# Performance work log

Hardware: AMD Instinct MI355X
Metric: run time of the kernel (lower is better)

Reference implementation:

```python
import jax, jax.numpy as jnp
import numpy as np
from jax.scipy.special import gammaln

BIG_NEG = -1e9
MAX_K = 20  # args.sm_max_span_length


def setup_inputs() -> dict:
    key = jax.random.key(0)
    ks = jax.random.split(key, 7)
    B, N, d, C = 16, 2048, 256, 128
    features = jax.random.normal(ks[0], (B, N, d), dtype=jnp.float32)
    lengths = jax.random.randint(ks[1], (B,), N // 2, N + 1)
    gaussian_means = jax.random.normal(ks[2], (C, d), dtype=jnp.float32)
    cov_diag = jax.random.uniform(ks[3], (d,), minval=0.5, maxval=1.5, dtype=jnp.float32)
    transition_logits = jax.random.normal(ks[4], (C, C), dtype=jnp.float32)
    init_logits = jax.random.uniform(ks[5], (C,), dtype=jnp.float32)
    poisson_log_rates = jax.random.normal(ks[6], (C,), dtype=jnp.float32) * 0.5 + 1.5
    return {"features": features, "lengths": lengths, "gaussian_means": gaussian_means,
            "cov_diag": cov_diag, "transition_logits": transition_logits,
            "init_logits": init_logits, "poisson_log_rates": poisson_log_rates}


def _emission_log_probs(features, means, cov_diag):
    # Diagonal-covariance MultivariateNormal log-prob, one class per column.
    # Quadratic form expanded to avoid materializing [B,N,C,d].
    inv_var = 1.0 / cov_diag
    d = features.shape[-1]
    const = -0.5 * (d * jnp.log(2.0 * jnp.pi) + jnp.sum(jnp.log(cov_diag)))
    xq = jnp.einsum('bnd,d->bn', features * features, inv_var)          # [B,N]
    mq = jnp.einsum('cd,d->c', means * means, inv_var)                  # [C]
    xm = jnp.einsum('bnd,cd->bnc', features, means * inv_var)           # [B,N,C]
    return const - 0.5 * (xq[..., None] + mq[None, None, :] - 2.0 * xm)  # [B,N,C]


def _length_log_probs(log_rates, K):
    # Poisson log-prob for span lengths k = 1..K.
    ks = jnp.arange(1, K + 1, dtype=jnp.float32)[:, None]               # [K,1]
    return ks * log_rates[None, :] - jnp.exp(log_rates)[None, :] - gammaln(ks + 1.0)  # [K,C]


def _transition_log_probs(transition_logits):
    C = transition_logits.shape[0]
    masked = jnp.where(jnp.eye(C, dtype=bool), BIG_NEG, transition_logits)  # no self-transitions
    return jax.nn.log_softmax(masked, axis=0)  # normalized over destination class (dim 0)


def _semimarkov_logZ(emis_lp, lengths, init_lp, trans_lp, len_lp, K):
    # Segmental (semi-Markov) CRF forward algorithm with sliding-window span sums.
    B, N, C = emis_lp.shape
    cum = jnp.concatenate([jnp.zeros((B, 1, C), emis_lp.dtype), jnp.cumsum(emis_lp, axis=1)], axis=1)
    cum_pad = jnp.concatenate([jnp.zeros((B, K, C), emis_lp.dtype), cum], axis=1)  # idx t+K <-> position t
    beta0 = jnp.full((B, N + 1 + K, C), BIG_NEG, emis_lp.dtype)
    beta0 = beta0.at[:, K, :].set(init_lp[None, :])  # position 0: initial distribution
    len_rev = len_lp[::-1]  # len_rev[j] == length log-prob of span length K-j

    def step(beta, t):
        w = jax.lax.dynamic_slice(beta, (0, t, 0), (B, K, C))        # beta at positions t-K..t-1
        cw = jax.lax.dynamic_slice(cum_pad, (0, t, 0), (B, K, C))
        ct = jax.lax.dynamic_slice(cum_pad, (0, t + K, 0), (B, 1, C))
        span = w + len_rev[None, :, :] + (ct - cw)                    # [B,K,C] span scores ending at t
        alpha_t = jax.nn.logsumexp(span, axis=1)                      # [B,C]
        beta_t = jax.nn.logsumexp(alpha_t[:, None, :] + trans_lp[None, :, :], axis=2)  # to-class
        beta = jax.lax.dynamic_update_slice(beta, beta_t[:, None, :], (0, t + K, 0))
        return beta, alpha_t

    _, alphas = jax.lax.scan(step, beta0, jnp.arange(1, N + 1))       # alphas: [N,B,C]
    final = alphas[lengths - 1, jnp.arange(B)]                        # [B,C] at each sequence end
    return jax.nn.logsumexp(final, axis=1)                            # [B] log partition


def reference(features, lengths, gaussian_means, cov_diag, transition_logits, init_logits, poisson_log_rates):
    emis_lp = _emission_log_probs(features, gaussian_means, cov_diag)
    init_lp = jax.nn.log_softmax(init_logits, axis=0)
    trans_lp = _transition_log_probs(transition_logits)
    len_lp = _length_log_probs(poisson_log_rates, MAX_K)
    return _semimarkov_logZ(emis_lp, lengths, init_lp, trans_lp, len_lp, MAX_K)
```

## Files before the change

### kernel.cpp

```cpp
#include <hip/hip_runtime.h>
#include <math.h>

#define Bb 16
#define Nn 2048
#define Dd 256
#define Cc 128
#define Kk 20
#define BIG_NEG -1.0e9f

#define WS_EMIS   0
#define WS_MSC    (WS_EMIS + Bb*Nn*Cc)
#define WS_XQ     (WS_MSC + Cc*Dd)
#define WS_ECHAN  (WS_XQ + Bb*Nn)
#define WS_T      (WS_ECHAN + Cc)
#define WS_LEN    (WS_T + Cc*Cc)
#define WS_INIT   (WS_LEN + Kk*Cc)
#define WS_IVAR   (WS_INIT + Cc)

typedef __attribute__((ext_vector_type(8))) short short8;
typedef __attribute__((ext_vector_type(4))) float float4v;

__device__ __forceinline__ unsigned short f32_to_bf16(float x) {
  unsigned int u = __builtin_bit_cast(unsigned int, x);
  u = (u + 0x7FFFu + ((u >> 16) & 1u)) >> 16;
  return (unsigned short)u;
}

#define DPP_STEP(x, op, ctrl, rmask)                                          \
  do {                                                                        \
    int _yi = __builtin_amdgcn_update_dpp(                                    \
        __builtin_bit_cast(int, x), __builtin_bit_cast(int, x), ctrl, rmask,  \
        0xF, true);                                                           \
    x = op(x, __builtin_bit_cast(float, _yi));                                \
  } while (0)

__device__ __forceinline__ float dpp_add(float a, float b) { return a + b; }

__device__ __forceinline__ float wave_max64(float x) {
  DPP_STEP(x, fmaxf, 0xB1, 0xF);
  DPP_STEP(x, fmaxf, 0x4E, 0xF);
  DPP_STEP(x, fmaxf, 0x141, 0xF);
  DPP_STEP(x, fmaxf, 0x140, 0xF);
  DPP_STEP(x, fmaxf, 0x142, 0xA);
  DPP_STEP(x, fmaxf, 0x143, 0xC);
  return __builtin_bit_cast(float,
      __builtin_amdgcn_readlane(__builtin_bit_cast(int, x), 63));
}

__device__ __forceinline__ float wave_sum64(float x) {
  DPP_STEP(x, dpp_add, 0xB1, 0xF);
  DPP_STEP(x, dpp_add, 0x4E, 0xF);
  DPP_STEP(x, dpp_add, 0x141, 0xF);
  DPP_STEP(x, dpp_add, 0x140, 0xF);
  DPP_STEP(x, dpp_add, 0x142, 0xA);
  DPP_STEP(x, dpp_add, 0x143, 0xC);
  return __builtin_bit_cast(float,
      __builtin_amdgcn_readlane(__builtin_bit_cast(int, x), 63));
}

__global__ void prep_kernel(const float* __restrict__ means,
                            const float* __restrict__ cov,
                            const float* __restrict__ tl,
                            const float* __restrict__ il,
                            const float* __restrict__ plr,
                            float* __restrict__ ws) {
  __shared__ float s_iv[Dd];
  __shared__ float s_red[4];
  __shared__ float s_tlse[Cc];
  int tid = threadIdx.x;

  float cv = cov[tid];
  float iv = 1.0f / cv;
  s_iv[tid] = iv;
  ws[WS_IVAR + tid] = iv;
  float lg = __logf(cv);
  #pragma unroll
  for (int off = 1; off < 64; off <<= 1) lg += __shfl_xor(lg, off, 64);
  if ((tid & 63) == 0) s_red[tid >> 6] = lg;
  __syncthreads();
  float logdet = s_red[0] + s_red[1] + s_red[2] + s_red[3];
  float cconst = -0.5f * ((float)Dd * 1.8378770664093453f + logdet);

  unsigned short* mscb = (unsigned short*)(ws + WS_MSC);
  for (int idx = tid; idx < Cc * Dd; idx += 256) {
    int d = idx & (Dd - 1);
    mscb[idx] = f32_to_bf16(means[idx] * s_iv[d]);
  }
  if (tid < Cc) {
    float acc = 0.0f;
    for (int d = 0; d < Dd; d++) {
      float m = means[tid * Dd + d];
      acc = fmaf(m * m, s_iv[d], acc);
    }
    ws[WS_ECHAN + tid] = cconst - 0.5f * acc;
  }
  for (int idx = tid; idx < Kk * Cc; idx += 256) {
    int L = idx / Cc + 1;
    int c = idx & (Cc - 1);
    float r = plr[c];
    ws[WS_LEN + idx] = (float)L * r - __expf(r) - lgammaf((float)(L + 1));
  }

  __syncthreads();
  float x = (tid < Cc) ? il[tid] : -INFINITY;
  float mx = x;
  #pragma unroll
  for (int off = 1; off < 64; off <<= 1) mx = fmaxf(mx, __shfl_xor(mx, off, 64));
  if ((tid & 63) == 0) s_red[tid >> 6] = mx;
  __syncthreads();
  float M = fmaxf(s_red[0], s_red[1]);
  float se = (tid < Cc) ? __expf(x - M) : 0.0f;
  #pragma unroll
  for (int off = 1; off < 64; off <<= 1) se += __shfl_xor(se, off, 64);
  __syncthreads();
  if ((tid & 63) == 0) s_red[tid >> 6] = se;
  __syncthreads();
  float lse = M + __logf(s_red[0] + s_red[1]);
  if (tid < Cc) ws[WS_INIT + tid] = x - lse;

  if (tid < Cc) {
    int j = tid;
    float m2 = -INFINITY;
    for (int i = 0; i < Cc; i++) if (i != j) m2 = fmaxf(m2, tl[i * Cc + j]);
    float s2 = 0.0f;
    for (int i = 0; i < Cc; i++) if (i != j) s2 += __expf(tl[i * Cc + j] - m2);
    s_tlse[j] = m2 + __logf(s2);
  }
  __syncthreads();
  for (int idx = tid; idx < Cc * Cc; idx += 256) {
    int i = idx / Cc;
    int j = idx & (Cc - 1);
    ws[WS_T + idx] = (i == j) ? 0.0f : __expf(tl[idx] - s_tlse[j]);
  }
}

__global__ void xq_kernel(const float* __restrict__ f, float* __restrict__ ws) {
  int pos = blockIdx.x * 4 + (threadIdx.x >> 6);
  int lane = threadIdx.x & 63;
  const float4 fv = *(const float4*)&f[(size_t)pos * Dd + lane * 4];
  const float4 vv = *(const float4*)&ws[WS_IVAR + lane * 4];
  float a = fv.x * fv.x * vv.x + fv.y * fv.y * vv.y +
            fv.z * fv.z * vv.z + fv.w * fv.w * vv.w;
  #pragma unroll
  for (int off = 1; off < 64; off <<= 1) a += __shfl_xor(a, off, 64);
  if (lane == 0) ws[WS_XQ + pos] = a;
}

__launch_bounds__(256)
__global__ void emis_mfma_kernel(const float* __restrict__ f, float* __restrict__ ws) {
  const unsigned short* msc = (const unsigned short*)(ws + WS_MSC);
  float* emis = ws + WS_EMIS;
  int tid = threadIdx.x;
  int w = tid >> 6, lane = tid & 63, g = lane >> 4, l16 = lane & 15;
  int b = blockIdx.x >> 6;
  int n0 = (blockIdx.x & 63) << 5;
  int c0 = w << 5;

  const float* fbase = f + (size_t)(b * Nn + n0) * Dd;
  float4v acc[2][2];
  #pragma unroll
  for (int rt = 0; rt < 2; rt++)
    #pragma unroll
    for (int ct = 0; ct < 2; ct++) acc[rt][ct] = (float4v){0.f, 0.f, 0.f, 0.f};

  #pragma unroll
  for (int k0 = 0; k0 < Dd; k0 += 32) {
    int kk = k0 + g * 8;
    short8 afr[2], bfr[2];
    #pragma unroll
    for (int rt = 0; rt < 2; rt++) {
      const float* src = fbase + (size_t)(rt * 16 + l16) * Dd + kk;
      float4 v0 = *(const float4*)src;
      float4 v1 = *(const float4*)(src + 4);
      short8 fr;
      fr[0] = (short)f32_to_bf16(v0.x); fr[1] = (short)f32_to_bf16(v0.y);
      fr[2] = (short)f32_to_bf16(v0.z); fr[3] = (short)f32_to_bf16(v0.w);
      fr[4] = (short)f32_to_bf16(v1.x); fr[5] = (short)f32_to_bf16(v1.y);
      fr[6] = (short)f32_to_bf16(v1.z); fr[7] = (short)f32_to_bf16(v1.w);
      afr[rt] = fr;
    }
    #pragma unroll
    for (int ct = 0; ct < 2; ct++)
      bfr[ct] = *(const short8*)&msc[(size_t)(c0 + ct * 16 + l16) * Dd + kk];
    #pragma unroll
    for (int rt = 0; rt < 2; rt++)
      #pragma unroll
      for (int ct = 0; ct < 2; ct++)
        acc[rt][ct] = __builtin_amdgcn_mfma_f32_16x16x32_bf16(afr[rt], bfr[ct], acc[rt][ct], 0, 0, 0);
  }

  #pragma unroll
  for (int rt = 0; rt < 2; rt++) {
    #pragma unroll
    for (int ct = 0; ct < 2; ct++) {
      int cc = c0 + ct * 16 + l16;
      float ec = ws[WS_ECHAN + cc];
      #pragma unroll
      for (int r = 0; r < 4; r++) {
        int row = rt * 16 + g * 4 + r;
        int nn = n0 + row;
        emis[(size_t)(b * Nn + nn) * Cc + cc] =
            ec - 0.5f * ws[WS_XQ + b * Nn + nn] + acc[rt][ct][r];
      }
    }
  }
}

__launch_bounds__(128, 1)
__global__ void scan_kernel(const int* __restrict__ lengths,
                            const float* __restrict__ ws,
                            float* __restrict__ out) {
  __shared__ __align__(16) unsigned short p_lds[2][Cc];
  __shared__ float lds_wv[2][2];
  __shared__ float lds_men[2][2][8];
  __shared__ float lds_out[2][2];

  int tid = threadIdx.x;
  int w = tid >> 6;
  int lane = tid & 63;
  int g = lane >> 4;
  int l15 = lane & 15;
  int c = w * 64 + lane;
  int b = blockIdx.x;
  int len_b = lengths[b];
  const float* emis = ws + WS_EMIS + (size_t)b * Nn * Cc;

  short8 Tf[4][4];
  {
    const float* T = ws + WS_T;
    #pragma unroll
    for (int nt = 0; nt < 4; nt++)
      #pragma unroll
      for (int kc = 0; kc < 4; kc++) {
        const float* src = &T[(size_t)((w * 4 + nt) * 16 + l15) * Cc + kc * 32 + g * 8];
        short8 fr;
        #pragma unroll
        for (int j = 0; j < 8; j++) fr[j] = (short)f32_to_bf16(src[j]);
        Tf[nt][kc] = fr;
      }
  }

  float elen[Kk];
  #pragma unroll
  for (int k = 0; k < Kk; k++) elen[k] = __expf(ws[WS_LEN + k * Cc + c]);
  float elen0 = elen[0];

  float E[Kk - 1];
  #pragma unroll
  for (int s = 0; s < Kk - 1; s++) E[s] = 0.0f;

  float q = __expf(ws[WS_INIT + c]);
  float Stail = 0.0f;
  float cum = 0.0f;
  float Dlt = 0.0f, dcomp = 0.0f;

  float e[8], en[8];
  #pragma unroll
  for (int j = 0; j < 8; j++) e[j] = emis[(size_t)j * Cc + c];
  #pragma unroll
  for (int j = 0; j < 8; j++) {
    float m = wave_max64(e[j]);
    if (lane == 0) lds_men[0][w][j] = m;
  }
  __syncthreads();
  float ee = __expf(e[0] - fmaxf(lds_men[0][0][0], lds_men[0][1][0]));

  bool done = false;
  for (int tg = 1; tg <= Nn && !done; tg += 8) {
    int gp = ((tg - 1) >> 3) & 1;
    #pragma unroll
    for (int i = 0; i < 8; i++) {
      int t = tg + i;
      int buf = t & 1;
      bool fin = (t == len_b);
      float ecur = e[i];
      float S = fmaf(q, elen0, Stail);
      float a = 0.0f;

      if (fin) {
        a = (cum + ecur) + Dlt + __logf(fmaxf(S, 1e-37f));
        float Mw = wave_max64(a);
        if (lane == 0) lds_out[0][w] = Mw;
      } else {
        float v = S * ee;
        p_lds[buf][c] = f32_to_bf16(v);
        float wvp = wave_max64(v);
        if (lane == 0) lds_wv[buf][w] = wvp;
      }
      __syncthreads();

      if (fin) {
        float Mb = fmaxf(lds_out[0][0], lds_out[0][1]);
        float ps = wave_sum64(__expf(a - Mb));
        if (lane == 0) lds_out[1][w] = ps;
        __syncthreads();
        if (tid == 0) out[b] = Mb + __logf(lds_out[1][0] + lds_out[1][1]);
        done = true;
        break;
      }

      short8 pa0 = *(const short8*)&p_lds[buf][g * 8];
      short8 pa1 = *(const short8*)&p_lds[buf][32 + g * 8];
      short8 pa2 = *(const short8*)&p_lds[buf][64 + g * 8];
      short8 pa3 = *(const short8*)&p_lds[buf][96 + g * 8];
      float wv = fmaxf(fmaxf(lds_wv[buf][0], lds_wv[buf][1]), 1.0e-30f);
      float r = __builtin_amdgcn_rcpf(wv);

      if (i == 0) {
        #pragma unroll
        for (int j = 0; j < 8; j++) {
          int rr = tg + 7 + j;
          if (rr > Nn - 1) rr = Nn - 1;
          en[j] = emis[(size_t)rr * Cc + c];
        }
      }

      float4v z = {0.0f, 0.0f, 0.0f, 0.0f};
      float qv[4];
      #pragma unroll
      for (int nt = 0; nt < 4; nt++) {
        float4v x = __builtin_amdgcn_mfma_f32_16x16x32_bf16(pa1, Tf[nt][1],
                      __builtin_amdgcn_mfma_f32_16x16x32_bf16(pa0, Tf[nt][0], z, 0, 0, 0),
                      0, 0, 0);
        float4v y = __builtin_amdgcn_mfma_f32_16x16x32_bf16(pa3, Tf[nt][3],
                      __builtin_amdgcn_mfma_f32_16x16x32_bf16(pa2, Tf[nt][2], z, 0, 0, 0),
                      0, 0, 0);
        qv[nt] = x[0] + y[0];
      }

      float sch = ee * r;
      #pragma unroll
      for (int s = Kk - 2; s >= 1; s--) E[s] = E[s - 1] * sch;
      E[0] = q * sch;

      float s0 = E[0] * elen[1];
      float s1 = E[1] * elen[2];
      float s2 = E[2] * elen[3];
      float s3 = E[3] * elen[4];
      s0 = fmaf(E[4], elen[5], s0);   s1 = fmaf(E[5], elen[6], s1);
      s2 = fmaf(E[6], elen[7], s2);   s3 = fmaf(E[7], elen[8], s3);
      s0 = fmaf(E[8], elen[9], s0);   s1 = fmaf(E[9], elen[10], s1);
      s2 = fmaf(E[10], elen[11], s2); s3 = fmaf(E[11], elen[12], s3);
      s0 = fmaf(E[12], elen[13], s0); s1 = fmaf(E[13], elen[14], s1);
      s2 = fmaf(E[14], elen[15], s2); s3 = fmaf(E[15], elen[16], s3);
      s0 = fmaf(E[16], elen[17], s0); s1 = fmaf(E[17], elen[18], s1);
      s2 = fmaf(E[18], elen[19], s2);
      Stail = (s0 + s1) + (s2 + s3);

      float meC = fmaxf(lds_men[gp][0][i], lds_men[gp][1][i]);
      float dla = meC + __logf(wv);
      {
        float dd = dla - ecur;
        float yk = dd - dcomp;
        float t2 = Dlt + yk;
        dcomp = (t2 - Dlt) - yk;
        Dlt = t2;
      }
      cum += ecur;

      if (i >= 2) {
        float m = wave_max64(en[i - 2]);
        if (lane == 0) lds_men[gp ^ 1][w][i - 2] = m;
      }
      if (i == 6) {
        float m = wave_max64(en[6]);
        if (lane == 0) lds_men[gp ^ 1][w][6] = m;
      }
      if (i == 7) {
        float m = wave_max64(en[7]);
        if (lane == 0) lds_men[gp ^ 1][w][7] = m;
      }

      if (i < 7) {
        float meN = fmaxf(lds_men[gp][0][i + 1], lds_men[gp][1][i + 1]);
        ee = __expf(e[i + 1] - meN);
      }

      float qs01 = (g & 1) ? qv[1] : qv[0];
      float qs23 = (g & 1) ? qv[3] : qv[2];
      float qs = (g & 2) ? qs23 : qs01;
      q = qs * r;
    }
    if (!done) {
      #pragma unroll
      for (int j = 0; j < 8; j++) e[j] = en[j];
      int gp = ((tg - 1) >> 3) & 1;
      float me0 = fmaxf(lds_men[gp ^ 1][0][0], lds_men[gp ^ 1][1][0]);
      ee = __expf(e[0] - me0);
    }
  }
}

extern "C" void kernel_launch(void* const* d_in, const int* in_sizes, int n_in,
                              void* d_out, int out_size, void* d_ws, size_t ws_size,
                              hipStream_t stream) {
  const float* features = (const float*)d_in[0];
  const int* lengths = (const int*)d_in[1];
  const float* means = (const float*)d_in[2];
  const float* cov = (const float*)d_in[3];
  const float* tl = (const float*)d_in[4];
  const float* il = (const float*)d_in[5];
  const float* plr = (const float*)d_in[6];
  float* out = (float*)d_out;
  float* ws = (float*)d_ws;

  prep_kernel<<<1, 256, 0, stream>>>(means, cov, tl, il, plr, ws);
  xq_kernel<<<(Bb * Nn) / 4, 256, 0, stream>>>(features, ws);
  emis_mfma_kernel<<<Bb * (Nn / 32), 256, 0, stream>>>(features, ws);
  scan_kernel<<<Bb, 128, 0, stream>>>(lengths, ws, out);
}
```

Measured before the change: 1.559 ms.

## Derive per-step normalizer from bf16 LDS fragments and defer rescale to next step

The scan no longer does a wave max reduction plus an LDS exchange for the normalizer each step. Each wave recomputes the max from the bf16 probability fragments it already reads for the MFMA, via packed u16 max and a short DPP tail. The reciprocal and log of that normalizer are folded into the next step's emission scale, which takes them off the critical path. __syncthreads is replaced by a raw s_waitcnt+s_barrier, bf16 conversion becomes plain truncation, and emission prefetch loads are spread across the 8 substeps. The risks are extra bf16 truncation error and rescaling that is delayed by one step.

```diff
diff --git a/kernel.cpp b/kernel.cpp
--- a/kernel.cpp
+++ b/kernel.cpp
@@ -19,6 +19,9 @@
 
 typedef __attribute__((ext_vector_type(8))) short short8;
 typedef __attribute__((ext_vector_type(4))) float float4v;
+typedef __attribute__((ext_vector_type(8))) unsigned short u16x8;
+typedef __attribute__((ext_vector_type(4))) unsigned short u16x4;
+typedef __attribute__((ext_vector_type(2))) unsigned short u16x2;
 
 __device__ __forceinline__ unsigned short f32_to_bf16(float x) {
   unsigned int u = __builtin_bit_cast(unsigned int, x);
@@ -56,6 +59,32 @@
   DPP_STEP(x, dpp_add, 0x143, 0xC);
   return __builtin_bit_cast(float,
       __builtin_amdgcn_readlane(__builtin_bit_cast(int, x), 63));
+}
+
+#define WAVE_BARRIER() asm volatile("s_waitcnt lgkmcnt(0)\n\ts_barrier" ::: "memory")
+
+__device__ __forceinline__ float frag_max_to_f32(short8 a, short8 b, short8 c, short8 d) {
+  u16x8 ua = __builtin_bit_cast(u16x8, a), ub = __builtin_bit_cast(u16x8, b);
+  u16x8 uc = __builtin_bit_cast(u16x8, c), ud = __builtin_bit_cast(u16x8, d);
+  u16x8 m8 = __builtin_elementwise_max(__builtin_elementwise_max(ua, ub),
+                                       __builtin_elementwise_max(uc, ud));
+  u16x4 lo4 = __builtin_shufflevector(m8, m8, 0, 1, 2, 3);
+  u16x4 hi4 = __builtin_shufflevector(m8, m8, 4, 5, 6, 7);
+  u16x4 m4 = __builtin_elementwise_max(lo4, hi4);
+  u16x2 lo2 = __builtin_shufflevector(m4, m4, 0, 1);
+  u16x2 hi2 = __builtin_shufflevector(m4, m4, 2, 3);
+  u16x2 m2 = __builtin_elementwise_max(lo2, hi2);
+  unsigned mm = (unsigned)m2[0];
+  unsigned m1 = (unsigned)m2[1];
+  mm = mm > m1 ? mm : m1;
+  {
+    int y = __builtin_amdgcn_update_dpp((int)mm, (int)mm, 0x142, 0xA, 0xF, true);
+    unsigned uy = (unsigned)y; mm = mm > uy ? mm : uy;
+    y = __builtin_amdgcn_update_dpp((int)mm, (int)mm, 0x143, 0xC, 0xF, true);
+    uy = (unsigned)y; mm = mm > uy ? mm : uy;
+  }
+  unsigned full = (unsigned)__builtin_amdgcn_readlane((int)mm, 63);
+  return __builtin_bit_cast(float, full << 16);
 }
 
 __global__ void prep_kernel(const float* __restrict__ means,
@@ -211,7 +240,6 @@
                             const float* __restrict__ ws,
                             float* __restrict__ out) {
   __shared__ __align__(16) unsigned short p_lds[2][Cc];
-  __shared__ float lds_wv[2][2];
   __shared__ float lds_men[2][2][8];
   __shared__ float lds_out[2][2];
 
@@ -253,6 +281,8 @@
   float Stail = 0.0f;
   float cum = 0.0f;
   float Dlt = 0.0f, dcomp = 0.0f;
+  float r = 1.0f;
+  float lwv = 0.0f;
 
   float e[8], en[8];
   #pragma unroll
@@ -262,8 +292,8 @@
     float m = wave_max64(e[j]);
     if (lane == 0) lds_men[0][w][j] = m;
   }
-  __syncthreads();
-  float ee = __expf(e[0] - fmaxf(lds_men[0][0][0], lds_men[0][1][0]));
+  WAVE_BARRIER();
+  float eesc = __expf(e[0] - fmaxf(lds_men[0][0][0], lds_men[0][1][0]));
 
   bool done = false;
   for (int tg = 1; tg <= Nn && !done; tg += 8) {
@@ -282,18 +312,17 @@
         float Mw = wave_max64(a);
         if (lane == 0) lds_out[0][w] = Mw;
       } else {
-        float v = S * ee;
-        p_lds[buf][c] = f32_to_bf16(v);
-        float wvp = wave_max64(v);
-        if (lane == 0) lds_wv[buf][w] = wvp;
-      }
-      __syncthreads();
+        float v = S * eesc;
+        p_lds[buf][c] =
+            (unsigned short)(__builtin_bit_cast(unsigned int, v) >> 16);
+      }
+      WAVE_BARRIER();
 
       if (fin) {
         float Mb = fmaxf(lds_out[0][0], lds_out[0][1]);
         float ps = wave_sum64(__expf(a - Mb));
         if (lane == 0) lds_out[1][w] = ps;
-        __syncthreads();
+        WAVE_BARRIER();
         if (tid == 0) out[b] = Mb + __logf(lds_out[1][0] + lds_out[1][1]);
         done = true;
         break;
@@ -303,17 +332,20 @@
       short8 pa1 = *(const short8*)&p_lds[buf][32 + g * 8];
       short8 pa2 = *(const short8*)&p_lds[buf][64 + g * 8];
       short8 pa3 = *(const short8*)&p_lds[buf][96 + g * 8];
-      float wv = fmaxf(fmaxf(lds_wv[buf][0], lds_wv[buf][1]), 1.0e-30f);
-      float r = __builtin_amdgcn_rcpf(wv);
 
       if (i == 0) {
-        #pragma unroll
-        for (int j = 0; j < 8; j++) {
-          int rr = tg + 7 + j;
-          if (rr > Nn - 1) rr = Nn - 1;
-          en[j] = emis[(size_t)rr * Cc + c];
-        }
-      }
+        int r0 = tg + 7;  if (r0 > Nn - 1) r0 = Nn - 1;
+        int r1 = tg + 8;  if (r1 > Nn - 1) r1 = Nn - 1;
+        int r2 = tg + 9;  if (r2 > Nn - 1) r2 = Nn - 1;
+        en[0] = emis[(size_t)r0 * Cc + c];
+        en[1] = emis[(size_t)r1 * Cc + c];
+        en[2] = emis[(size_t)r2 * Cc + c];
+      } else if (i <= 5) {
+        int rr = tg + 9 + i; if (rr > Nn - 1) rr = Nn - 1;
+        en[i + 2] = emis[(size_t)rr * Cc + c];
+      }
+
+      float wv = fmaxf(frag_max_to_f32(pa0, pa1, pa2, pa3), 1.0e-30f);
 
       float4v z = {0.0f, 0.0f, 0.0f, 0.0f};
       float qv[4];
@@ -328,10 +360,9 @@
         qv[nt] = x[0] + y[0];
       }
 
-      float sch = ee * r;
-      #pragma unroll
-      for (int s = Kk - 2; s >= 1; s--) E[s] = E[s - 1] * sch;
-      E[0] = q * sch;
+      #pragma unroll
+      for (int s = Kk - 2; s >= 1; s--) E[s] = E[s - 1] * eesc;
+      E[0] = q * eesc;
 
       float s0 = E[0] * elen[1];
       float s1 = E[1] * elen[2];
@@ -348,7 +379,7 @@
       Stail = (s0 + s1) + (s2 + s3);
 
       float meC = fmaxf(lds_men[gp][0][i], lds_men[gp][1][i]);
-      float dla = meC + __logf(wv);
+      float dla = meC + lwv;
       {
         float dd = dla - ecur;
         float yk = dd - dcomp;
@@ -358,6 +389,9 @@
       }
       cum += ecur;
 
+      r = __builtin_amdgcn_rcpf(wv);
+      lwv = __logf(wv);
+
       if (i >= 2) {
         float m = wave_max64(en[i - 2]);
         if (lane == 0) lds_men[gp ^ 1][w][i - 2] = m;
@@ -373,20 +407,20 @@
 
       if (i < 7) {
         float meN = fmaxf(lds_men[gp][0][i + 1], lds_men[gp][1][i + 1]);
-        ee = __expf(e[i + 1] - meN);
+        eesc = __expf(e[i + 1] - meN) * r;
       }
 
       float qs01 = (g & 1) ? qv[1] : qv[0];
       float qs23 = (g & 1) ? qv[3] : qv[2];
       float qs = (g & 2) ? qs23 : qs01;
-      q = qs * r;
+      q = qs;
     }
     if (!done) {
       #pragma unroll
       for (int j = 0; j < 8; j++) e[j] = en[j];
       int gp = ((tg - 1) >> 3) & 1;
       float me0 = fmaxf(lds_men[gp ^ 1][0][0], lds_men[gp ^ 1][1][0]);
-      ee = __expf(e[0] - me0);
+      eesc = __expf(e[0] - me0) * r;
     }
   }
 }
```

Measured after the change: 1.588 ms. No clear change (+1.8%).
